# Kernel tuning notes

Measured on AMD Instinct MI355X. Metric: run time of the kernel, lower is better.

The kernel has to match this reference:

```python
import jax, jax.numpy as jnp
import numpy as np

BS = 4096
FD = 768   # feature_dim
PD = 500   # proj_dim
ZD = 300   # z_dim
R = 10     # retrieval_num
U = 10     # retrieval_user_num
N_PER = 3 + 2 * R + U  # 33 nodes per sample


def _lin(x, w, b):
    return x @ w.T + b


def _build_incidence(bs, r, u):
    # Faithful to get_hyper_edge_index_and_weight: 4 group edges per sample
    # plus R pair edges that (as in the original code) omit the batch bias,
    # i.e. always reference sample-0 nodes. dhg.Hypergraph dedups duplicate
    # edges, so the R pair edges appear once.
    n = 3 + 2 * r + u
    node_list, edge_list = [], []
    e = 0
    for b in range(bs):
        o = b * n
        groups = [
            list(range(o, o + 3)),
            list(range(o + 3, o + 3 + r)) + [o],
            list(range(o + 3 + r, o + 3 + 2 * r)) + [o + 1],
            list(range(o + 3 + 2 * r, o + n)) + [o + 2],
        ]
        for g in groups:
            node_list.extend(g)
            edge_list.extend([e] * len(g))
            e += 1
    for i in range(r):
        node_list.extend([3 + i, 3 + r + i])
        edge_list.extend([e, e])
        e += 1
    return np.asarray(node_list, np.int32), np.asarray(edge_list, np.int32), e


def setup_inputs() -> dict:
    key = jax.random.key(0)
    ks = jax.random.split(key, 32)

    def rn(k, shape, s=1.0):
        return jax.random.normal(k, shape, dtype=jnp.float32) * s

    inp = {
        "visual_feature": rn(ks[0], (BS, 1, FD)),
        "textual_feature": rn(ks[1], (BS, 1, FD)),
        "similarity": rn(ks[2], (BS, R)),
        "retrieved_visual_feature": rn(ks[3], (BS, R, 1, FD)),
        "retrieved_textual_feature": rn(ks[4], (BS, R, FD)),
        "retrieved_label": jax.random.uniform(ks[5], (BS, R, 1), dtype=jnp.float32),
        "user": rn(ks[6], (BS, FD)),
        "retrieved_user": rn(ks[7], (BS, U, FD)),
        "retrieved_user_similarity": rn(ks[8], (BS, U)),
        # learned params (0.02-scaled normal init)
        "vis_w": rn(ks[9], (PD, FD), 0.02), "vis_b": jnp.zeros((PD,), jnp.float32),
        "txt_w": rn(ks[10], (PD, FD), 0.02), "txt_b": jnp.zeros((PD,), jnp.float32),
        "usr_w": rn(ks[11], (PD, FD), 0.02), "usr_b": jnp.zeros((PD,), jnp.float32),
        "rvis_w": rn(ks[12], (PD, FD), 0.02), "rvis_b": jnp.zeros((PD,), jnp.float32),
        "rtxt_w": rn(ks[13], (PD, FD), 0.02), "rtxt_b": jnp.zeros((PD,), jnp.float32),
        "rusr_w": rn(ks[14], (PD, FD), 0.02), "rusr_b": jnp.zeros((PD,), jnp.float32),
        "hg_w": rn(ks[15], (ZD, PD), 0.02), "hg_b": jnp.zeros((ZD,), jnp.float32),
        "lbl_w": rn(ks[16], (ZD, 1), 0.02), "lbl_b": jnp.zeros((ZD,), jnp.float32),
        "p1_w": rn(ks[17], (800, ZD * 7), 0.02), "p1_b": jnp.zeros((800,), jnp.float32),
        "p2_w": rn(ks[18], (200, 800), 0.02), "p2_b": jnp.zeros((200,), jnp.float32),
        "p3_w": rn(ks[19], (1, 200), 0.02), "p3_b": jnp.zeros((1,), jnp.float32),
    }
    return inp


def reference(visual_feature, textual_feature, similarity, retrieved_visual_feature,
              retrieved_textual_feature, retrieved_label, user, retrieved_user,
              retrieved_user_similarity,
              vis_w, vis_b, txt_w, txt_b, usr_w, usr_b,
              rvis_w, rvis_b, rtxt_w, rtxt_b, rusr_w, rusr_b,
              hg_w, hg_b, lbl_w, lbl_b,
              p1_w, p1_b, p2_w, p2_b, p3_w, p3_b):
    bs = visual_feature.shape[0]
    # dense tanh embeddings -> per-sample node feature block [bs, 33, 500]
    t = jnp.tanh(_lin(textual_feature, txt_w, txt_b))
    v = jnp.tanh(_lin(visual_feature, vis_w, vis_b))
    u = jnp.tanh(_lin(user[:, None, :], usr_w, usr_b))
    rt = jnp.tanh(_lin(retrieved_textual_feature, rtxt_w, rtxt_b))
    rv = jnp.tanh(_lin(retrieved_visual_feature[:, :, 0, :], rvis_w, rvis_b))
    ru = jnp.tanh(_lin(retrieved_user, rusr_w, rusr_b))
    X = jnp.concatenate([t, v, u, rt, rv, ru], axis=1).reshape(-1, PD)  # [bs*33, 500]

    # hypergraph conv (HGNN+ layer, softmax_then_sum over unit incidence == mean)
    node_ids, edge_ids, E = _build_incidence(bs, R, U)  # static, built at trace time
    N = X.shape[0]
    Xt = _lin(X, hg_w, hg_b)  # theta: [N, 300]
    ones = jnp.ones(node_ids.shape[0], jnp.float32)
    deg_e = jax.ops.segment_sum(ones, edge_ids, num_segments=E)
    Y = jax.ops.segment_sum(Xt[node_ids], edge_ids, num_segments=E) / deg_e[:, None]
    deg_v = jax.ops.segment_sum(ones, node_ids, num_segments=N)
    Xo = jax.ops.segment_sum(Y[edge_ids], node_ids, num_segments=N) / deg_v[:, None]
    Xo = jax.nn.relu(Xo).reshape(bs, N_PER, ZD)

    # retrieval aggregation: softmax-weighted sums over retrieved sets
    sim = jax.nn.softmax(similarity, axis=1)                      # [bs, R]
    usim = jax.nn.softmax(retrieved_user_similarity, axis=1)      # [bs, U]
    rt_agg = jnp.einsum('br,brd->bd', sim, Xo[:, 3:3 + R, :])
    rv_agg = jnp.einsum('br,brd->bd', sim, Xo[:, 3 + R:3 + 2 * R, :])
    ru_agg = jnp.einsum('br,brd->bd', usim, Xo[:, 3 + 2 * R:3 + 2 * R + U, :])
    lbl_agg = jnp.einsum('br,bro->bo', sim, retrieved_label)      # [bs, 1]
    lbl_emb = jax.nn.relu(_lin(lbl_agg, lbl_w, lbl_b))            # [bs, 300]

    feat = jnp.concatenate(
        [Xo[:, 0, :], Xo[:, 1, :], Xo[:, 2, :], rv_agg, rt_agg, ru_agg, lbl_emb], axis=1)
    h = jax.nn.relu(_lin(feat, p1_w, p1_b))
    h = jax.nn.relu(_lin(h, p2_w, p2_b))
    out = jax.nn.sigmoid(_lin(h, p3_w, p3_b))  # [bs, 1]
    return out
```

## Files before the change

kernel.cpp:

```cpp
#include <hip/hip_runtime.h>
#include <math.h>

#define BS 4096
#define FD 768
#define PD 500
#define ZD 300
#define RNUM 10

typedef short bf16x8 __attribute__((ext_vector_type(8)));
typedef float f32x4 __attribute__((ext_vector_type(4)));

__device__ __forceinline__ unsigned int fbits(float f) {
  union { float f; unsigned int u; } v; v.f = f; return v.u;
}

__device__ __forceinline__ unsigned int pack2bf(float f0, float f1) {
  unsigned int u0 = fbits(f0) + 0x8000u;
  unsigned int u1 = fbits(f1) + 0x8000u;
  return __builtin_amdgcn_perm(u1, u0, 0x07060302u);
}

#define BM 128
#define BN 64
#define BK 16
#define TM 8
#define TN 4
template <int ACT>
__global__ __launch_bounds__(256) void gemm_kernel(
    const float* __restrict__ A, const float* __restrict__ W,
    const float* __restrict__ bias, float* __restrict__ C,
    int M, int N, int K) {
  __shared__ float As[BK][BM + 4];
  __shared__ float Bs[BK][BN + 4];
  const int m0 = blockIdx.x * BM;
  const int n0 = blockIdx.y * BN;
  const int tid = threadIdx.x;
  const int tx = tid & 15;
  const int ty = tid >> 4;
  float acc[TM][TN];
#pragma unroll
  for (int i = 0; i < TM; i++)
#pragma unroll
    for (int j = 0; j < TN; j++) acc[i][j] = 0.f;
  const int l_row = tid >> 2;
  const int l_k4 = (tid & 3) * 4;
  for (int k0 = 0; k0 < K; k0 += BK) {
#pragma unroll
    for (int half = 0; half < 2; ++half) {
      int m = m0 + l_row + half * 64;
      int k = k0 + l_k4;
      float4 v = make_float4(0.f, 0.f, 0.f, 0.f);
      if (m < M && k + 4 <= K) v = *(const float4*)(A + (size_t)m * K + k);
      As[l_k4 + 0][l_row + half * 64] = v.x;
      As[l_k4 + 1][l_row + half * 64] = v.y;
      As[l_k4 + 2][l_row + half * 64] = v.z;
      As[l_k4 + 3][l_row + half * 64] = v.w;
    }
    {
      int n = n0 + l_row;
      int k = k0 + l_k4;
      float4 v = make_float4(0.f, 0.f, 0.f, 0.f);
      if (n < N && k + 4 <= K) v = *(const float4*)(W + (size_t)n * K + k);
      Bs[l_k4 + 0][l_row] = v.x;
      Bs[l_k4 + 1][l_row] = v.y;
      Bs[l_k4 + 2][l_row] = v.z;
      Bs[l_k4 + 3][l_row] = v.w;
    }
    __syncthreads();
#pragma unroll
    for (int k = 0; k < BK; k++) {
      float a[TM], b[TN];
#pragma unroll
      for (int i = 0; i < TM; i++) a[i] = As[k][ty * TM + i];
#pragma unroll
      for (int j = 0; j < TN; j++) b[j] = Bs[k][tx * TN + j];
#pragma unroll
      for (int i = 0; i < TM; i++)
#pragma unroll
        for (int j = 0; j < TN; j++) acc[i][j] += a[i] * b[j];
    }
    __syncthreads();
  }
#pragma unroll
  for (int i = 0; i < TM; i++) {
    int m = m0 + ty * TM + i;
    if (m >= M) continue;
#pragma unroll
    for (int j = 0; j < TN; j++) {
      int n = n0 + tx * TN + j;
      if (n >= N) continue;
      float v = acc[i][j] + bias[n];
      if (ACT == 1) v = fmaxf(v, 0.f);
      C[(size_t)m * N + n] = v;
    }
  }
}

__global__ __launch_bounds__(256) void padcast(
    const float* __restrict__ src, unsigned short* __restrict__ dst,
    int rs, int cs, int rd, int cd) {
  int i = blockIdx.x * 256 + threadIdx.x;
  if (i >= rd * cd) return;
  int r = i / cd, c = i - r * cd;
  float v = (r < rs && c < cs) ? src[(size_t)r * cs + c] : 0.f;
  dst[i] = (unsigned short)((fbits(v) + 0x8000u) >> 16);
}


template <int ACT>
__global__ __launch_bounds__(256) void mfma_gemm(
    const float* __restrict__ A, int lda, int Ka,
    const unsigned short* __restrict__ B, int Kp,
    const float* __restrict__ bias, float* __restrict__ C, int Nout) {
  __shared__ unsigned short ldsA[128 * 32];
  __shared__ unsigned short ldsB[128 * 32];
  const int tid = threadIdx.x;
  const int n0 = blockIdx.x * 128;
  const int m0 = blockIdx.y * 128;

  const int arow = tid >> 1;
  const int ahalf = (tid & 1) << 4;
  const int ag = (tid & 1) << 1;
  const int aswz = (arow >> 1) & 3;
  unsigned short* awp0 = &ldsA[((size_t)arow * 4 + ((ag | 0) ^ aswz)) * 8];
  unsigned short* awp1 = &ldsA[((size_t)arow * 4 + ((ag | 1) ^ aswz)) * 8];
  const float* aptr = A + (size_t)(m0 + arow) * lda;

  unsigned short* bwp0 = &ldsB[((size_t)arow * 4 + ((ag | 0) ^ aswz)) * 8];
  unsigned short* bwp1 = &ldsB[((size_t)arow * 4 + ((ag | 1) ^ aswz)) * 8];
  const unsigned short* bptr = B + (size_t)(n0 + arow) * Kp + ag * 8;

  const int lane = tid & 63;
  const int wave = tid >> 6;
  const int wm = (wave >> 1) << 6;
  const int wn = (wave & 1) << 6;
  const int r16 = lane & 15;
  const int kq = lane >> 4;

  const unsigned short* afp[4];
  const unsigned short* bfp[4];
#pragma unroll
  for (int i = 0; i < 4; i++) {
    int rowA = wm + i * 16 + r16;
    afp[i] = &ldsA[((size_t)rowA * 4 + (kq ^ ((rowA >> 1) & 3))) * 8];
    int rowB = wn + i * 16 + r16;
    bfp[i] = &ldsB[((size_t)rowB * 4 + (kq ^ ((rowB >> 1) & 3))) * 8];
  }

  f32x4 acc[4][4] = {};

  for (int k0 = 0; k0 < Kp; k0 += 32) {
    float4 f[4];
#pragma unroll
    for (int q = 0; q < 4; q++) {
      int k = k0 + ahalf + q * 4;
      if (k < Ka) f[q] = *(const float4*)(aptr + k);
      else f[q] = make_float4(0.f, 0.f, 0.f, 0.f);
    }
    uint4 w0, w1;
    w0.x = pack2bf(f[0].x, f[0].y); w0.y = pack2bf(f[0].z, f[0].w);
    w0.z = pack2bf(f[1].x, f[1].y); w0.w = pack2bf(f[1].z, f[1].w);
    w1.x = pack2bf(f[2].x, f[2].y); w1.y = pack2bf(f[2].z, f[2].w);
    w1.z = pack2bf(f[3].x, f[3].y); w1.w = pack2bf(f[3].z, f[3].w);
    uint4 bv0 = *(const uint4*)(bptr + k0);
    uint4 bv1 = *(const uint4*)(bptr + k0 + 8);
    *(uint4*)awp0 = w0;
    *(uint4*)awp1 = w1;
    *(uint4*)bwp0 = bv0;
    *(uint4*)bwp1 = bv1;
    __syncthreads();
    bf16x8 a[4], b[4];
#pragma unroll
    for (int i = 0; i < 4; i++) a[i] = *(const bf16x8*)afp[i];
#pragma unroll
    for (int i = 0; i < 4; i++) b[i] = *(const bf16x8*)bfp[i];
#pragma unroll
    for (int i = 0; i < 4; i++)
#pragma unroll
      for (int j = 0; j < 4; j++)
        acc[i][j] = __builtin_amdgcn_mfma_f32_16x16x32_bf16(a[i], b[j], acc[i][j], 0, 0, 0);
    __syncthreads();
  }

#pragma unroll
  for (int j = 0; j < 4; j++) {
    int n = n0 + wn + j * 16 + r16;
    if (n >= Nout) continue;
    float bi = bias[n];
#pragma unroll
    for (int i = 0; i < 4; i++) {
#pragma unroll
      for (int r = 0; r < 4; r++) {
        int m = m0 + wm + i * 16 + kq * 4 + r;
        float v = acc[i][j][r] + bi;
        if (ACT == 1) v = fmaxf(v, 0.f);
        C[(size_t)m * Nout + n] = v;
      }
    }
  }
}

struct EmbedArgs {
  const float* A[6];
  const float* bias[6];
};

__global__ __launch_bounds__(256) void embed_mfma(
    EmbedArgs ea, const unsigned short* __restrict__ Wbf,
    float* __restrict__ S, float* __restrict__ E0) {
  __shared__ unsigned short ldsA[128 * 32];
  __shared__ unsigned short ldsB[128 * 32];
  const int tid = threadIdx.x;
  const int n0 = blockIdx.x * 128;
  const int m0 = blockIdx.y * 128;

  int g, base;
  if (m0 < 4096) { g = 0; base = 0; }
  else if (m0 < 8192) { g = 1; base = 4096; }
  else if (m0 < 12288) { g = 2; base = 8192; }
  else if (m0 < 53248) { g = 3; base = 12288; }
  else if (m0 < 94208) { g = 4; base = 53248; }
  else { g = 5; base = 94208; }

  const int arow = tid >> 1;
  const int ahalf = (tid & 1) << 4;
  const int ag = (tid & 1) << 1;
  const int aswz = (arow >> 1) & 3;
  unsigned short* awp0 = &ldsA[((size_t)arow * 4 + ((ag | 0) ^ aswz)) * 8];
  unsigned short* awp1 = &ldsA[((size_t)arow * 4 + ((ag | 1) ^ aswz)) * 8];
  const float* aptr = ea.A[g] + (size_t)(m0 - base + arow) * FD;

  unsigned short* bwp0 = &ldsB[((size_t)arow * 4 + ((ag | 0) ^ aswz)) * 8];
  unsigned short* bwp1 = &ldsB[((size_t)arow * 4 + ((ag | 1) ^ aswz)) * 8];
  const unsigned short* bptr =
      Wbf + (size_t)g * 512 * FD + (size_t)(n0 + arow) * FD + ag * 8;

  const int lane = tid & 63;
  const int wave = tid >> 6;
  const int wm = (wave >> 1) << 6;
  const int wn = (wave & 1) << 6;
  const int r16 = lane & 15;
  const int kq = lane >> 4;

  const unsigned short* afp[4];
  const unsigned short* bfp[4];
#pragma unroll
  for (int i = 0; i < 4; i++) {
    int rowA = wm + i * 16 + r16;
    afp[i] = &ldsA[((size_t)rowA * 4 + (kq ^ ((rowA >> 1) & 3))) * 8];
    int rowB = wn + i * 16 + r16;
    bfp[i] = &ldsB[((size_t)rowB * 4 + (kq ^ ((rowB >> 1) & 3))) * 8];
  }

  f32x4 acc[4][4] = {};

  for (int k0 = 0; k0 < FD; k0 += 32) {
    float4 f[4];
#pragma unroll
    for (int q = 0; q < 4; q++) f[q] = *(const float4*)(aptr + k0 + ahalf + q * 4);
    uint4 w0, w1;
    w0.x = pack2bf(f[0].x, f[0].y); w0.y = pack2bf(f[0].z, f[0].w);
    w0.z = pack2bf(f[1].x, f[1].y); w0.w = pack2bf(f[1].z, f[1].w);
    w1.x = pack2bf(f[2].x, f[2].y); w1.y = pack2bf(f[2].z, f[2].w);
    w1.z = pack2bf(f[3].x, f[3].y); w1.w = pack2bf(f[3].z, f[3].w);
    uint4 bv0 = *(const uint4*)(bptr + k0);
    uint4 bv1 = *(const uint4*)(bptr + k0 + 8);
    *(uint4*)awp0 = w0;
    *(uint4*)awp1 = w1;
    *(uint4*)bwp0 = bv0;
    *(uint4*)bwp1 = bv1;
    __syncthreads();
    bf16x8 a[4], b[4];
#pragma unroll
    for (int i = 0; i < 4; i++) a[i] = *(const bf16x8*)afp[i];
#pragma unroll
    for (int i = 0; i < 4; i++) b[i] = *(const bf16x8*)bfp[i];
#pragma unroll
    for (int i = 0; i < 4; i++)
#pragma unroll
      for (int j = 0; j < 4; j++)
        acc[i][j] = __builtin_amdgcn_mfma_f32_16x16x32_bf16(a[i], b[j], acc[i][j], 0, 0, 0);
    __syncthreads();
  }

  const float* bias = ea.bias[g];
#pragma unroll
  for (int j = 0; j < 4; j++) {
    int n = n0 + wn + j * 16 + r16;
    if (n >= PD) continue;
    float bi = bias[n];
#pragma unroll
    for (int i = 0; i < 4; i++) {
#pragma unroll
      for (int r = 0; r < 4; r++) {
        int m = m0 + wm + i * 16 + kq * 4 + r;
        int rl = m - base;
        float v = tanhf(acc[i][j][r] + bi);
        if (g < 3) {
          S[((size_t)g * BS + rl) * PD + n] = v;
        } else {
          int bb = rl / 10;
          int rr = rl - bb * 10;
          atomicAdd(&S[((size_t)g * BS + bb) * PD + n], v);
          if (g != 5 && bb == 0) E0[((size_t)(g - 3) * 10 + rr) * PD + n] = v;
        }
      }
    }
  }
}

__global__ __launch_bounds__(256) void means_kernel(
    const float* __restrict__ S, float* __restrict__ Mn) {
  const int total = 4 * BS * PD;
  for (int i = blockIdx.x * blockDim.x + threadIdx.x; i < total;
       i += gridDim.x * blockDim.x) {
    int m = i / PD;
    int k = i - m * PD;
    int b = m >> 2, e = m & 3;
    float v;
    const size_t o = (size_t)b * PD + k;
    if (e == 0)
      v = (S[o] + S[(size_t)BS * PD + o] + S[2 * (size_t)BS * PD + o]) * (1.f / 3.f);
    else if (e == 1)
      v = (S[3 * (size_t)BS * PD + o] + S[o]) * (1.f / 11.f);
    else if (e == 2)
      v = (S[4 * (size_t)BS * PD + o] + S[(size_t)BS * PD + o]) * (1.f / 11.f);
    else
      v = (S[5 * (size_t)BS * PD + o] + S[2 * (size_t)BS * PD + o]) * (1.f / 11.f);
    Mn[i] = v;
  }
}

__global__ __launch_bounds__(256) void xte_kernel(
    const float* __restrict__ E0, const float* __restrict__ hg_w,
    const float* __restrict__ hg_b, float* __restrict__ XtE) {
  const int i = blockIdx.x;
  __shared__ float row[PD];
  for (int k = threadIdx.x; k < PD; k += 256) row[k] = E0[(size_t)i * PD + k];
  __syncthreads();
  for (int n = threadIdx.x; n < ZD; n += 256) {
    float s = 0.f;
    const float* w = hg_w + (size_t)n * PD;
    for (int k = 0; k < PD; k++) s += row[k] * w[k];
    XtE[(size_t)i * ZD + n] = s + hg_b[n];
  }
}

__global__ __launch_bounds__(256) void feat_kernel(
    const float* __restrict__ Y, const float* __restrict__ XtE,
    const float* __restrict__ sim_in, const float* __restrict__ label,
    const float* __restrict__ lbl_w, const float* __restrict__ lbl_b,
    float* __restrict__ feat) {
  const int b = blockIdx.x;
  __shared__ float w[RNUM];
  __shared__ float lbl_agg_s;
  if (threadIdx.x == 0) {
    float s[RNUM], mx = -1e30f;
    for (int r = 0; r < RNUM; r++) {
      s[r] = sim_in[(size_t)b * RNUM + r];
      mx = fmaxf(mx, s[r]);
    }
    float sum = 0.f;
    for (int r = 0; r < RNUM; r++) { s[r] = expf(s[r] - mx); sum += s[r]; }
    float la = 0.f;
    for (int r = 0; r < RNUM; r++) {
      w[r] = s[r] / sum;
      la += w[r] * label[(size_t)b * RNUM + r];
    }
    lbl_agg_s = la;
  }
  __syncthreads();
  const float* Yb = Y + (size_t)b * 4 * ZD;
  float* fb = feat + (size_t)b * 7 * ZD;
  const float la = lbl_agg_s;
  for (int n = threadIdx.x; n < ZD; n += blockDim.x) {
    float y0 = Yb[n], y1 = Yb[ZD + n], y2 = Yb[2 * ZD + n], y3 = Yb[3 * ZD + n];
    fb[n] = fmaxf(0.5f * (y0 + y1), 0.f);
    fb[ZD + n] = fmaxf(0.5f * (y0 + y2), 0.f);
    fb[2 * ZD + n] = fmaxf(0.5f * (y0 + y3), 0.f);
    float rv, rt;
    if (b == 0) {
      rv = 0.f; rt = 0.f;
      for (int r = 0; r < RNUM; r++) {
        float yp = 0.5f * (XtE[(size_t)r * ZD + n] + XtE[(size_t)(10 + r) * ZD + n]);
        rt += w[r] * fmaxf(0.5f * (y1 + yp), 0.f);
        rv += w[r] * fmaxf(0.5f * (y2 + yp), 0.f);
      }
    } else {
      rt = fmaxf(y1, 0.f);
      rv = fmaxf(y2, 0.f);
    }
    fb[3 * ZD + n] = rv;
    fb[4 * ZD + n] = rt;
    fb[5 * ZD + n] = fmaxf(y3, 0.f);
    fb[6 * ZD + n] = fmaxf(la * lbl_w[n] + lbl_b[n], 0.f);
  }
}

__global__ __launch_bounds__(256) void head_kernel(
    const float* __restrict__ h2, const float* __restrict__ p3_w,
    const float* __restrict__ p3_b, float* __restrict__ out) {
  const int wave = (blockIdx.x * blockDim.x + threadIdx.x) >> 6;
  const int lane = threadIdx.x & 63;
  if (wave >= BS) return;
  const float* row = h2 + (size_t)wave * 200;
  float s = 0.f;
  for (int k = lane; k < 200; k += 64) s += row[k] * p3_w[k];
#pragma unroll
  for (int off = 32; off; off >>= 1) s += __shfl_down(s, off, 64);
  if (lane == 0) out[wave] = 1.f / (1.f + expf(-(s + p3_b[0])));
}

extern "C" void kernel_launch(void* const* d_in, const int* in_sizes, int n_in,
                              void* d_out, int out_size, void* d_ws,
                              size_t ws_size, hipStream_t stream) {
  (void)in_sizes; (void)n_in; (void)out_size; (void)ws_size;

  const float* visual = (const float*)d_in[0];
  const float* textual = (const float*)d_in[1];
  const float* similarity = (const float*)d_in[2];
  const float* r_visual = (const float*)d_in[3];
  const float* r_textual = (const float*)d_in[4];
  const float* r_label = (const float*)d_in[5];
  const float* user = (const float*)d_in[6];
  const float* r_user = (const float*)d_in[7];
  const float* vis_w = (const float*)d_in[9];
  const float* vis_b = (const float*)d_in[10];
  const float* txt_w = (const float*)d_in[11];
  const float* txt_b = (const float*)d_in[12];
  const float* usr_w = (const float*)d_in[13];
  const float* usr_b = (const float*)d_in[14];
  const float* rvis_w = (const float*)d_in[15];
  const float* rvis_b = (const float*)d_in[16];
  const float* rtxt_w = (const float*)d_in[17];
  const float* rtxt_b = (const float*)d_in[18];
  const float* rusr_w = (const float*)d_in[19];
  const float* rusr_b = (const float*)d_in[20];
  const float* hg_w = (const float*)d_in[21];
  const float* hg_b = (const float*)d_in[22];
  const float* lbl_w = (const float*)d_in[23];
  const float* lbl_b = (const float*)d_in[24];
  const float* p1_w = (const float*)d_in[25];
  const float* p1_b = (const float*)d_in[26];
  const float* p2_w = (const float*)d_in[27];
  const float* p2_b = (const float*)d_in[28];
  const float* p3_w = (const float*)d_in[29];
  const float* p3_b = (const float*)d_in[30];
  float* out = (float*)d_out;

  float* ws = (float*)d_ws;
  float* S = ws;
  float* E0 = S + (size_t)6 * BS * PD;
  float* XtE = E0 + 20 * PD;
  float* Mn = XtE + 20 * ZD;
  float* Y = Mn + (size_t)4 * BS * PD;
  float* feat = Y + (size_t)4 * BS * ZD;
  float* h1 = feat + (size_t)BS * 7 * ZD;
  float* h2 = h1 + (size_t)BS * 800;
  unsigned short* Wbf = (unsigned short*)(h2 + (size_t)BS * 200);
  unsigned short* hgwbf = Wbf + (size_t)6 * 512 * FD;
  unsigned short* p1wbf = hgwbf + (size_t)384 * 512;

  const float* ew[6] = {txt_w, vis_w, usr_w, rtxt_w, rvis_w, rusr_w};
  for (int g = 0; g < 6; g++) {
    padcast<<<(512 * FD + 255) / 256, 256, 0, stream>>>(
        ew[g], Wbf + (size_t)g * 512 * FD, PD, FD, 512, FD);
  }
  padcast<<<(384 * 512 + 255) / 256, 256, 0, stream>>>(hg_w, hgwbf, ZD, PD, 384, 512);
  padcast<<<(896 * 2112 + 255) / 256, 256, 0, stream>>>(p1_w, p1wbf, 800, 2100, 896, 2112);

  hipMemsetAsync(S + (size_t)3 * BS * PD, 0, (size_t)3 * BS * PD * sizeof(float),
                 stream);

  EmbedArgs ea;
  ea.A[0] = textual;  ea.bias[0] = txt_b;
  ea.A[1] = visual;   ea.bias[1] = vis_b;
  ea.A[2] = user;     ea.bias[2] = usr_b;
  ea.A[3] = r_textual; ea.bias[3] = rtxt_b;
  ea.A[4] = r_visual;  ea.bias[4] = rvis_b;
  ea.A[5] = r_user;    ea.bias[5] = rusr_b;

  embed_mfma<<<dim3(4, 135168 / 128), 256, 0, stream>>>(ea, Wbf, S, E0);
  xte_kernel<<<20, 256, 0, stream>>>(E0, hg_w, hg_b, XtE);
  means_kernel<<<4096, 256, 0, stream>>>(S, Mn);
  mfma_gemm<0><<<dim3(3, 16384 / 128), 256, 0, stream>>>(
      Mn, PD, PD, hgwbf, 512, hg_b, Y, ZD);
  feat_kernel<<<BS, 256, 0, stream>>>(Y, XtE, similarity, r_label, lbl_w, lbl_b,
                                      feat);
  mfma_gemm<1><<<dim3(7, BS / 128), 256, 0, stream>>>(
      feat, 2100, 2100, p1wbf, 2112, p1_b, h1, 800);
  gemm_kernel<1><<<dim3(BS / BM, (200 + BN - 1) / BN), 256, 0, stream>>>(
      h1, p2_w, p2_b, h2, BS, 200, 800);
  head_kernel<<<BS * 64 / 256, 256, 0, stream>>>(h2, p3_w, p3_b, out);
}
```

Measured before the change: 1.300 ms.

## Double-buffer GEMM LDS tiles and widen embed tiles with LDS segment reduction

Both MFMA GEMM kernels now use double-buffered LDS with register prefetch of the next K tile, so there is one barrier per iteration instead of two. The embed kernel switches to 512-thread blocks that cover all 512 output columns per row tile. The A activations are therefore read and bf16-converted once rather than four times. The per-sample sum over 10 retrieved rows now goes through an LDS reduction with mostly plain stores, replacing per-element global atomics. The cost is more registers and LDS per block, which may lower occupancy, plus a more complex epilogue with extra barriers.

```diff
diff --git a/kernel.cpp b/kernel.cpp
--- a/kernel.cpp
+++ b/kernel.cpp
@@ -106,14 +106,13 @@
   dst[i] = (unsigned short)((fbits(v) + 0x8000u) >> 16);
 }
 
-
 template <int ACT>
 __global__ __launch_bounds__(256) void mfma_gemm(
     const float* __restrict__ A, int lda, int Ka,
     const unsigned short* __restrict__ B, int Kp,
     const float* __restrict__ bias, float* __restrict__ C, int Nout) {
-  __shared__ unsigned short ldsA[128 * 32];
-  __shared__ unsigned short ldsB[128 * 32];
+  __shared__ unsigned short ldsA[2][128 * 32];
+  __shared__ unsigned short ldsB[2][128 * 32];
   const int tid = threadIdx.x;
   const int n0 = blockIdx.x * 128;
   const int m0 = blockIdx.y * 128;
@@ -122,13 +121,10 @@
   const int ahalf = (tid & 1) << 4;
   const int ag = (tid & 1) << 1;
   const int aswz = (arow >> 1) & 3;
-  unsigned short* awp0 = &ldsA[((size_t)arow * 4 + ((ag | 0) ^ aswz)) * 8];
-  unsigned short* awp1 = &ldsA[((size_t)arow * 4 + ((ag | 1) ^ aswz)) * 8];
+  const int aw0 = (arow * 4 + ((ag | 0) ^ aswz)) * 8;
+  const int aw1 = (arow * 4 + ((ag | 1) ^ aswz)) * 8;
   const float* aptr = A + (size_t)(m0 + arow) * lda;
-
-  unsigned short* bwp0 = &ldsB[((size_t)arow * 4 + ((ag | 0) ^ aswz)) * 8];
-  unsigned short* bwp1 = &ldsB[((size_t)arow * 4 + ((ag | 1) ^ aswz)) * 8];
-  const unsigned short* bptr = B + (size_t)(n0 + arow) * Kp + ag * 8;
+  const unsigned short* bptr = B + (size_t)(n0 + arow) * Kp + ahalf;
 
   const int lane = tid & 63;
   const int wave = tid >> 6;
@@ -137,49 +133,76 @@
   const int r16 = lane & 15;
   const int kq = lane >> 4;
 
-  const unsigned short* afp[4];
-  const unsigned short* bfp[4];
+  int afoff[4], bfoff[4];
 #pragma unroll
   for (int i = 0; i < 4; i++) {
     int rowA = wm + i * 16 + r16;
-    afp[i] = &ldsA[((size_t)rowA * 4 + (kq ^ ((rowA >> 1) & 3))) * 8];
+    afoff[i] = (rowA * 4 + (kq ^ ((rowA >> 1) & 3))) * 8;
     int rowB = wn + i * 16 + r16;
-    bfp[i] = &ldsB[((size_t)rowB * 4 + (kq ^ ((rowB >> 1) & 3))) * 8];
+    bfoff[i] = (rowB * 4 + (kq ^ ((rowB >> 1) & 3))) * 8;
   }
 
   f32x4 acc[4][4] = {};
-
-  for (int k0 = 0; k0 < Kp; k0 += 32) {
-    float4 f[4];
-#pragma unroll
-    for (int q = 0; q < 4; q++) {
-      int k = k0 + ahalf + q * 4;
-      if (k < Ka) f[q] = *(const float4*)(aptr + k);
-      else f[q] = make_float4(0.f, 0.f, 0.f, 0.f);
-    }
+  const int NT = Kp >> 5;
+
+  float4 f[4];
+  uint4 bv0, bv1;
+#pragma unroll
+  for (int q = 0; q < 4; q++) {
+    int k = ahalf + q * 4;
+    f[q] = (k < Ka) ? *(const float4*)(aptr + k) : make_float4(0.f, 0.f, 0.f, 0.f);
+  }
+  bv0 = *(const uint4*)(bptr + 0);
+  bv1 = *(const uint4*)(bptr + 8);
+  {
     uint4 w0, w1;
     w0.x = pack2bf(f[0].x, f[0].y); w0.y = pack2bf(f[0].z, f[0].w);
     w0.z = pack2bf(f[1].x, f[1].y); w0.w = pack2bf(f[1].z, f[1].w);
     w1.x = pack2bf(f[2].x, f[2].y); w1.y = pack2bf(f[2].z, f[2].w);
     w1.z = pack2bf(f[3].x, f[3].y); w1.w = pack2bf(f[3].z, f[3].w);
-    uint4 bv0 = *(const uint4*)(bptr + k0);
-    uint4 bv1 = *(const uint4*)(bptr + k0 + 8);
-    *(uint4*)awp0 = w0;
-    *(uint4*)awp1 = w1;
-    *(uint4*)bwp0 = bv0;
-    *(uint4*)bwp1 = bv1;
-    __syncthreads();
+    *(uint4*)&ldsA[0][aw0] = w0;
+    *(uint4*)&ldsA[0][aw1] = w1;
+    *(uint4*)&ldsB[0][aw0] = bv0;
+    *(uint4*)&ldsB[0][aw1] = bv1;
+  }
+
+#pragma unroll 2
+  for (int t = 0; t < NT; ++t) {
+    const int cb = t & 1;
+    asm volatile("s_waitcnt lgkmcnt(0)" ::: "memory");
+    __builtin_amdgcn_s_barrier();
+    if (t + 1 < NT) {
+      const int k0 = (t + 1) << 5;
+#pragma unroll
+      for (int q = 0; q < 4; q++) {
+        int k = k0 + ahalf + q * 4;
+        f[q] = (k < Ka) ? *(const float4*)(aptr + k)
+                        : make_float4(0.f, 0.f, 0.f, 0.f);
+      }
+      bv0 = *(const uint4*)(bptr + k0);
+      bv1 = *(const uint4*)(bptr + k0 + 8);
+    }
     bf16x8 a[4], b[4];
 #pragma unroll
-    for (int i = 0; i < 4; i++) a[i] = *(const bf16x8*)afp[i];
-#pragma unroll
-    for (int i = 0; i < 4; i++) b[i] = *(const bf16x8*)bfp[i];
+    for (int i = 0; i < 4; i++) a[i] = *(const bf16x8*)&ldsA[cb][afoff[i]];
+#pragma unroll
+    for (int i = 0; i < 4; i++) b[i] = *(const bf16x8*)&ldsB[cb][bfoff[i]];
 #pragma unroll
     for (int i = 0; i < 4; i++)
 #pragma unroll
       for (int j = 0; j < 4; j++)
         acc[i][j] = __builtin_amdgcn_mfma_f32_16x16x32_bf16(a[i], b[j], acc[i][j], 0, 0, 0);
-    __syncthreads();
+    if (t + 1 < NT) {
+      uint4 w0, w1;
+      w0.x = pack2bf(f[0].x, f[0].y); w0.y = pack2bf(f[0].z, f[0].w);
+      w0.z = pack2bf(f[1].x, f[1].y); w0.w = pack2bf(f[1].z, f[1].w);
+      w1.x = pack2bf(f[2].x, f[2].y); w1.y = pack2bf(f[2].z, f[2].w);
+      w1.z = pack2bf(f[3].x, f[3].y); w1.w = pack2bf(f[3].z, f[3].w);
+      *(uint4*)&ldsA[cb ^ 1][aw0] = w0;
+      *(uint4*)&ldsA[cb ^ 1][aw1] = w1;
+      *(uint4*)&ldsB[cb ^ 1][aw0] = bv0;
+      *(uint4*)&ldsB[cb ^ 1][aw1] = bv1;
+    }
   }
 
 #pragma unroll
@@ -205,14 +228,13 @@
   const float* bias[6];
 };
 
-__global__ __launch_bounds__(256) void embed_mfma(
+__global__ __launch_bounds__(512, 2) void embed_mfma(
     EmbedArgs ea, const unsigned short* __restrict__ Wbf,
     float* __restrict__ S, float* __restrict__ E0) {
-  __shared__ unsigned short ldsA[128 * 32];
-  __shared__ unsigned short ldsB[128 * 32];
+  __shared__ unsigned short ldsA[2][128 * 32];
+  __shared__ unsigned short ldsB[2][512 * 32];
   const int tid = threadIdx.x;
-  const int n0 = blockIdx.x * 128;
-  const int m0 = blockIdx.y * 128;
+  const int m0 = blockIdx.x * 128;
 
   int g, base;
   if (m0 < 4096) { g = 0; base = 0; }
@@ -222,90 +244,155 @@
   else if (m0 < 94208) { g = 4; base = 53248; }
   else { g = 5; base = 94208; }
 
-  const int arow = tid >> 1;
-  const int ahalf = (tid & 1) << 4;
-  const int ag = (tid & 1) << 1;
+  const int arow = tid >> 2;
+  const int aq = tid & 3;
   const int aswz = (arow >> 1) & 3;
-  unsigned short* awp0 = &ldsA[((size_t)arow * 4 + ((ag | 0) ^ aswz)) * 8];
-  unsigned short* awp1 = &ldsA[((size_t)arow * 4 + ((ag | 1) ^ aswz)) * 8];
-  const float* aptr = ea.A[g] + (size_t)(m0 - base + arow) * FD;
-
-  unsigned short* bwp0 = &ldsB[((size_t)arow * 4 + ((ag | 0) ^ aswz)) * 8];
-  unsigned short* bwp1 = &ldsB[((size_t)arow * 4 + ((ag | 1) ^ aswz)) * 8];
-  const unsigned short* bptr =
-      Wbf + (size_t)g * 512 * FD + (size_t)(n0 + arow) * FD + ag * 8;
+  const int awoff = (arow * 4 + (aq ^ aswz)) * 8;
+  const float* aptr = ea.A[g] + (size_t)(m0 - base + arow) * FD + aq * 8;
+
+  const int brow = tid;
+  const int bswz = (brow >> 1) & 3;
+  int bwoff[4];
+#pragma unroll
+  for (int q = 0; q < 4; q++) bwoff[q] = (brow * 4 + (q ^ bswz)) * 8;
+  const unsigned short* bptr = Wbf + (size_t)g * 512 * FD + (size_t)brow * FD;
 
   const int lane = tid & 63;
   const int wave = tid >> 6;
-  const int wm = (wave >> 1) << 6;
-  const int wn = (wave & 1) << 6;
+  const int wm = (wave >> 2) << 6;
+  const int wn = (wave & 3) << 7;
   const int r16 = lane & 15;
   const int kq = lane >> 4;
 
-  const unsigned short* afp[4];
-  const unsigned short* bfp[4];
+  int afoff[4], bfoff[8];
 #pragma unroll
   for (int i = 0; i < 4; i++) {
     int rowA = wm + i * 16 + r16;
-    afp[i] = &ldsA[((size_t)rowA * 4 + (kq ^ ((rowA >> 1) & 3))) * 8];
-    int rowB = wn + i * 16 + r16;
-    bfp[i] = &ldsB[((size_t)rowB * 4 + (kq ^ ((rowB >> 1) & 3))) * 8];
-  }
-
-  f32x4 acc[4][4] = {};
-
-  for (int k0 = 0; k0 < FD; k0 += 32) {
-    float4 f[4];
-#pragma unroll
-    for (int q = 0; q < 4; q++) f[q] = *(const float4*)(aptr + k0 + ahalf + q * 4);
-    uint4 w0, w1;
-    w0.x = pack2bf(f[0].x, f[0].y); w0.y = pack2bf(f[0].z, f[0].w);
-    w0.z = pack2bf(f[1].x, f[1].y); w0.w = pack2bf(f[1].z, f[1].w);
-    w1.x = pack2bf(f[2].x, f[2].y); w1.y = pack2bf(f[2].z, f[2].w);
-    w1.z = pack2bf(f[3].x, f[3].y); w1.w = pack2bf(f[3].z, f[3].w);
-    uint4 bv0 = *(const uint4*)(bptr + k0);
-    uint4 bv1 = *(const uint4*)(bptr + k0 + 8);
-    *(uint4*)awp0 = w0;
-    *(uint4*)awp1 = w1;
-    *(uint4*)bwp0 = bv0;
-    *(uint4*)bwp1 = bv1;
-    __syncthreads();
-    bf16x8 a[4], b[4];
-#pragma unroll
-    for (int i = 0; i < 4; i++) a[i] = *(const bf16x8*)afp[i];
-#pragma unroll
-    for (int i = 0; i < 4; i++) b[i] = *(const bf16x8*)bfp[i];
+    afoff[i] = (rowA * 4 + (kq ^ ((rowA >> 1) & 3))) * 8;
+  }
+#pragma unroll
+  for (int j = 0; j < 8; j++) {
+    int rowB = wn + j * 16 + r16;
+    bfoff[j] = (rowB * 4 + (kq ^ ((rowB >> 1) & 3))) * 8;
+  }
+
+  f32x4 acc[4][8] = {};
+
+  float4 fa0 = *(const float4*)(aptr + 0);
+  float4 fa1 = *(const float4*)(aptr + 4);
+  uint4 bv[4];
+#pragma unroll
+  for (int q = 0; q < 4; q++) bv[q] = *(const uint4*)(bptr + q * 8);
+  {
+    uint4 aw;
+    aw.x = pack2bf(fa0.x, fa0.y); aw.y = pack2bf(fa0.z, fa0.w);
+    aw.z = pack2bf(fa1.x, fa1.y); aw.w = pack2bf(fa1.z, fa1.w);
+    *(uint4*)&ldsA[0][awoff] = aw;
+#pragma unroll
+    for (int q = 0; q < 4; q++) *(uint4*)&ldsB[0][bwoff[q]] = bv[q];
+  }
+
+  const int NT = FD / 32;
+#pragma unroll 2
+  for (int t = 0; t < NT; ++t) {
+    const int cb = t & 1;
+    asm volatile("s_waitcnt lgkmcnt(0)" ::: "memory");
+    __builtin_amdgcn_s_barrier();
+    if (t + 1 < NT) {
+      const float* ap = aptr + (t + 1) * 32;
+      fa0 = *(const float4*)(ap + 0);
+      fa1 = *(const float4*)(ap + 4);
+      const unsigned short* bp = bptr + (t + 1) * 32;
+#pragma unroll
+      for (int q = 0; q < 4; q++) bv[q] = *(const uint4*)(bp + q * 8);
+    }
+    bf16x8 a[4], b[8];
+#pragma unroll
+    for (int i = 0; i < 4; i++) a[i] = *(const bf16x8*)&ldsA[cb][afoff[i]];
+#pragma unroll
+    for (int j = 0; j < 8; j++) b[j] = *(const bf16x8*)&ldsB[cb][bfoff[j]];
 #pragma unroll
     for (int i = 0; i < 4; i++)
 #pragma unroll
-      for (int j = 0; j < 4; j++)
+      for (int j = 0; j < 8; j++)
         acc[i][j] = __builtin_amdgcn_mfma_f32_16x16x32_bf16(a[i], b[j], acc[i][j], 0, 0, 0);
-    __syncthreads();
+    if (t + 1 < NT) {
+      uint4 aw;
+      aw.x = pack2bf(fa0.x, fa0.y); aw.y = pack2bf(fa0.z, fa0.w);
+      aw.z = pack2bf(fa1.x, fa1.y); aw.w = pack2bf(fa1.z, fa1.w);
+      *(uint4*)&ldsA[cb ^ 1][awoff] = aw;
+#pragma unroll
+      for (int q = 0; q < 4; q++) *(uint4*)&ldsB[cb ^ 1][bwoff[q]] = bv[q];
+    }
   }
 
   const float* bias = ea.bias[g];
-#pragma unroll
-  for (int j = 0; j < 4; j++) {
-    int n = n0 + wn + j * 16 + r16;
-    if (n >= PD) continue;
-    float bi = bias[n];
-#pragma unroll
-    for (int i = 0; i < 4; i++) {
-#pragma unroll
-      for (int r = 0; r < 4; r++) {
-        int m = m0 + wm + i * 16 + kq * 4 + r;
-        int rl = m - base;
-        float v = tanhf(acc[i][j][r] + bi);
-        if (g < 3) {
-          S[((size_t)g * BS + rl) * PD + n] = v;
-        } else {
-          int bb = rl / 10;
-          int rr = rl - bb * 10;
-          atomicAdd(&S[((size_t)g * BS + bb) * PD + n], v);
-          if (g != 5 && bb == 0) E0[((size_t)(g - 3) * 10 + rr) * PD + n] = v;
+  if (g < 3) {
+#pragma unroll
+    for (int j = 0; j < 8; j++) {
+      int n = wn + j * 16 + r16;
+      if (n >= PD) continue;
+      float bi = bias[n];
+#pragma unroll
+      for (int i = 0; i < 4; i++) {
+#pragma unroll
+        for (int r = 0; r < 4; r++) {
+          int rl = m0 - base + wm + i * 16 + kq * 4 + r;
+          S[((size_t)g * BS + rl) * PD + n] = tanhf(acc[i][j][r] + bi);
         }
       }
     }
+    return;
+  }
+
+  const int R0 = m0 - base;
+  const int b0 = R0 / 10;
+  const int b1 = (R0 + 127) / 10;
+  const int ng = b1 - b0 + 1;
+  float* red = (float*)&ldsB[0][0];
+  const int myc = wave & 3;
+  __syncthreads();
+  for (int ch = 0; ch < 8; ++ch) {
+    if ((ch >> 1) == myc) {
+#pragma unroll
+      for (int jj = 0; jj < 4; jj++) {
+        int j = ((ch & 1) << 2) + jj;
+        int n = wn + j * 16 + r16;
+        int cl = (jj << 4) + r16;
+        float bi = (n < PD) ? bias[n] : 0.f;
+#pragma unroll
+        for (int i = 0; i < 4; i++) {
+#pragma unroll
+          for (int r = 0; r < 4; r++) {
+            int row = wm + i * 16 + kq * 4 + r;
+            red[row * 68 + cl] = acc[i][j][r] + bi;
+          }
+        }
+      }
+    }
+    __syncthreads();
+    for (int task = tid; task < ng * 64; task += 512) {
+      int cl = task & 63;
+      int bb = b0 + (task >> 6);
+      int n = (ch << 6) + cl;
+      if (n < PD) {
+        int rlo = bb * 10 - R0;
+        int rhi = rlo + 9;
+        int lo = rlo < 0 ? 0 : rlo;
+        int hi = rhi > 127 ? 127 : rhi;
+        float s = 0.f;
+        for (int r = lo; r <= hi; r++) s += tanhf(red[r * 68 + cl]);
+        size_t idx = ((size_t)g * BS + bb) * PD + n;
+        if (hi - lo == 9) S[idx] = s;
+        else atomicAdd(&S[idx], s);
+        if (g != 5 && bb == 0 && R0 == 0) {
+#pragma unroll
+          for (int rr = 0; rr < 10; rr++)
+            E0[((size_t)(g - 3) * 10 + rr) * PD + n] = tanhf(red[rr * 68 + cl]);
+        }
+      }
+    }
+    __syncthreads();
   }
 }
 
@@ -480,7 +567,7 @@
   ea.A[4] = r_visual;  ea.bias[4] = rvis_b;
   ea.A[5] = r_user;    ea.bias[5] = rusr_b;
 
-  embed_mfma<<<dim3(4, 135168 / 128), 256, 0, stream>>>(ea, Wbf, S, E0);
+  embed_mfma<<<dim3(135168 / 128), 512, 0, stream>>>(ea, Wbf, S, E0);
   xte_kernel<<<20, 256, 0, stream>>>(E0, hg_w, hg_b, XtE);
   means_kernel<<<4096, 256, 0, stream>>>(S, Mn);
   mfma_gemm<0><<<dim3(3, 16384 / 128), 256, 0, stream>>>(
```

Result: no change. 1.313 ms (+1.0%).
